# Kernel optimization log

Measured on AMD Instinct MI355X. Metric: run time of the kernel, lower is better.

## Reference

```python
import jax, jax.numpy as jnp
import numpy as np

T, B, D = 512, 16, 1024


def entmax_1_5(x):
    # x: [..., D] fp32. 1.5-entmax via sort + cumsum threshold search.
    x = x - jnp.max(x, axis=-1, keepdims=True)
    x_sorted = jnp.sort(x, axis=-1)[..., ::-1]          # descending
    cumsum = jnp.cumsum(x_sorted, axis=-1)
    d = x.shape[-1]
    k = jnp.arange(1, d + 1, dtype=x.dtype)
    tau = (cumsum - 1.0) / k                             # [..., D]
    support = x_sorted >= tau
    k_star = jnp.clip(jnp.sum(support, axis=-1, keepdims=True), 1, None)
    tau_star = jnp.take_along_axis(tau, k_star - 1, axis=-1)
    p_unnorm = jnp.sqrt(jnp.clip(x - tau_star, 0.0, None))  # (.)**0.5
    return p_unnorm / (jnp.sum(p_unnorm, axis=-1, keepdims=True) + 1e-10)


def setup_inputs() -> dict:
    key = jax.random.key(0)
    k1, k2, k3, k4 = jax.random.split(key, 4)
    x = jax.random.normal(k1, (T, B, D), dtype=jnp.float32)
    z = jax.random.normal(k2, (T, B, D), dtype=jnp.float32)
    h0 = jnp.zeros((B, D), dtype=jnp.float32)
    # parameters (xavier-ish scale for W_x, scaled near-orthogonal-ish for W_h)
    W_x = jax.random.normal(k3, (D, D), dtype=jnp.float32) * (1.0 / np.sqrt(D))
    W_h = jax.random.normal(k4, (D, D), dtype=jnp.float32) * (0.9 / np.sqrt(D))
    b = jnp.zeros((D,), dtype=jnp.float32)
    return {"x": x, "z": z, "h0": h0, "W_x": W_x, "W_h": W_h, "b": b}


def reference(x, z, h0, W_x, W_h, b):
    # gate does not depend on the recurrence -> compute for all T at once
    gate = entmax_1_5(z.astype(jnp.float32)).astype(z.dtype)  # [T,B,D]

    def step(h_prev, x_t):
        h_new = jnp.tanh(x_t @ W_x.T + h_prev @ W_h.T + b)
        return h_new, h_new

    _, hs = jax.lax.scan(step, h0, x)          # hs: [T,B,D]
    h = jnp.concatenate([h0[None], hs], axis=0)  # [T+1,B,D]
    output = hs * gate                           # [T,B,D]
    return (output, h)
```

## Files before the change

kernel.cpp:

```cpp
#include <hip/hip_runtime.h>
#include <math.h>

#define T_STEPS 512
#define BATCH   16
#define DIM     1024
#define M_TOTAL (T_STEPS*BATCH)
#define OUT_SEC ((size_t)M_TOTAL*DIM)
#define BD      (BATCH*DIM)

#define TAG_BYTES ((size_t)2*BD*8)

#define NB_GEMM 512
#define NB_GATE 2048

__device__ __forceinline__ float wred64(float v){
  #pragma unroll
  for (int off = 32; off >= 1; off >>= 1) v += __shfl_xor(v, off, 64);
  return v;
}

#define KA(v) asm volatile("" : "+v"(v.x), "+v"(v.y), "+v"(v.z), "+v"(v.w))

__global__ __launch_bounds__(256) void prep_kernel(const float* __restrict__ X,
                                                   const float* __restrict__ Wx,
                                                   const float* __restrict__ bias,
                                                   float* __restrict__ out_h,
                                                   const float* __restrict__ z,
                                                   float* __restrict__ gate_out){
  __shared__ float As[8][128];
  __shared__ float Bs[8][128];
  const int tid = threadIdx.x;

  if (blockIdx.x < NB_GEMM){
    const int bm = blockIdx.x >> 3;
    const int bn = blockIdx.x & 7;
    const int m0 = bm*128, n0 = bn*128;
    const int tx = tid & 15, ty = tid >> 4;
    const int sm = tid >> 1;
    const int sk = (tid & 1) * 4;

    float acc[8][8] = {};

    for (int k0 = 0; k0 < DIM; k0 += 8){
      const float4 av = *reinterpret_cast<const float4*>(
          X  + (size_t)(m0+sm)*DIM + k0 + sk);
      const float4 wv = *reinterpret_cast<const float4*>(
          Wx + (size_t)(n0+sm)*DIM + k0 + sk);
      __syncthreads();
      As[sk+0][sm]=av.x; As[sk+1][sm]=av.y; As[sk+2][sm]=av.z; As[sk+3][sm]=av.w;
      Bs[sk+0][sm]=wv.x; Bs[sk+1][sm]=wv.y; Bs[sk+2][sm]=wv.z; Bs[sk+3][sm]=wv.w;
      __syncthreads();
      #pragma unroll
      for (int k = 0; k < 8; ++k){
        float af[8], bf[8];
        #pragma unroll
        for (int i = 0; i < 8; ++i) af[i] = As[k][ty + 16*i];
        #pragma unroll
        for (int j = 0; j < 8; ++j) bf[j] = Bs[k][tx + 16*j];
        #pragma unroll
        for (int i = 0; i < 8; ++i)
          #pragma unroll
          for (int j = 0; j < 8; ++j) acc[i][j] = fmaf(af[i], bf[j], acc[i][j]);
      }
    }

    float bv[8];
    #pragma unroll
    for (int j = 0; j < 8; ++j) bv[j] = bias[n0 + tx + 16*j];
    #pragma unroll
    for (int i = 0; i < 8; ++i){
      float* dst = out_h + (size_t)(m0 + ty + 16*i + BATCH)*DIM + n0 + tx;
      #pragma unroll
      for (int j = 0; j < 8; ++j) dst[16*j] = acc[i][j] + bv[j];
    }
  } else {
    const int gb   = blockIdx.x - NB_GEMM;
    const int row  = gb * 4 + (tid >> 6);
    const int lane = tid & 63;
    const float* zr = z + (size_t)row * DIM;

    float x[16];
    #pragma unroll
    for (int e = 0; e < 4; ++e){
      float4 v = *reinterpret_cast<const float4*>(zr + e*256 + lane*4);
      x[e*4+0]=v.x; x[e*4+1]=v.y; x[e*4+2]=v.z; x[e*4+3]=v.w;
    }

    float m = x[0];
    #pragma unroll
    for (int i = 1; i < 16; ++i) m = fmaxf(m, x[i]);
    #pragma unroll
    for (int off = 32; off >= 1; off >>= 1) m = fmaxf(m, __shfl_xor(m, off, 64));

    float lo = m - 1.0f, hi = m;
    for (int it = 0; it < 30; ++it){
      float mid = 0.5f*(lo + hi);
      float f = 0.f;
      #pragma unroll
      for (int i = 0; i < 16; ++i) f += fmaxf(x[i] - mid, 0.f);
      f = wred64(f);
      if (f >= 1.0f) lo = mid; else hi = mid;
    }
    float s = 0.f, kc = 0.f;
    #pragma unroll
    for (int i = 0; i < 16; ++i){ if (x[i] > lo){ s += x[i]; kc += 1.f; } }
    s = wred64(s); kc = wred64(kc);
    const float tau = (s - 1.0f) / kc;

    float p[16]; float ps = 0.f;
    #pragma unroll
    for (int i = 0; i < 16; ++i){ p[i] = sqrtf(fmaxf(x[i] - tau, 0.f)); ps += p[i]; }
    ps = wred64(ps);
    const float inv = 1.0f / (ps + 1e-10f);

    float* go = gate_out + (size_t)row * DIM;
    #pragma unroll
    for (int e = 0; e < 4; ++e){
      float4 v; v.x=p[e*4]*inv; v.y=p[e*4+1]*inv; v.z=p[e*4+2]*inv; v.w=p[e*4+3]*inv;
      *reinterpret_cast<float4*>(go + e*256 + lane*4) = v;
    }
  }
}

__global__ __launch_bounds__(1024, 1) void rnn_tag(const float* __restrict__ h0,
                                                   const float* __restrict__ Wh,
                                                   float* __restrict__ out,
                                                   uint2* __restrict__ tagbuf){
  float* out_h = out + OUT_SEC;
  const int tid  = threadIdx.x;
  const int lane = tid & 63;
  const int w    = tid >> 6;
  const int b    = blockIdx.x >> 4;
  const int s    = blockIdx.x & 15;
  const int dbase = s*64 + w*4;

  __shared__ float hbuf[2][DIM];

  float4 wreg[4][4];
  #pragma unroll
  for (int r = 0; r < 4; ++r)
    #pragma unroll
    for (int j = 0; j < 4; ++j)
      wreg[r][j] = *reinterpret_cast<const float4*>(
          Wh + (size_t)(dbase + r)*DIM + lane*4 + j*256);

  KA(wreg[0][0]); KA(wreg[0][1]); KA(wreg[0][2]); KA(wreg[0][3]);
  KA(wreg[1][0]); KA(wreg[1][1]); KA(wreg[1][2]); KA(wreg[1][3]);
  KA(wreg[2][0]); KA(wreg[2][1]); KA(wreg[2][2]); KA(wreg[2][3]);
  KA(wreg[3][0]); KA(wreg[3][1]); KA(wreg[3][2]); KA(wreg[3][3]);

  if (tid < 16)
    reinterpret_cast<float4*>(out_h + (size_t)b*DIM + s*64)[tid] =
        reinterpret_cast<const float4*>(h0 + (size_t)b*DIM + s*64)[tid];

  const int  myrow  = 2*((lane >> 5) & 1) + ((lane >> 4) & 1);
  const bool active = ((lane & 15) == 0);

  for (int t = 0; t < T_STEPS; ++t){
    float pre_v = 0.f, gate_v = 0.f;
    if (active){
      const size_t d = dbase + myrow;
      pre_v  = out_h[(size_t)(t+1)*BD + (size_t)b*DIM + d];
      gate_v = out  [(size_t)t*BD     + (size_t)b*DIM + d];
    }

    if (t == 0){
      hbuf[0][tid] = h0[(size_t)b*DIM + tid];
    } else {
      const uint2* pp = tagbuf + (size_t)(t & 1)*BD + (size_t)b*DIM + tid;
      const unsigned want = (unsigned)t;
      uint2 q;
      do {
        asm volatile("global_load_dwordx2 %0, %1, off sc0 sc1\n\t"
                     "s_waitcnt vmcnt(0)"
                     : "=&v"(q) : "v"(pp) : "memory");
      } while (q.y != want);
      hbuf[t & 1][tid] = __uint_as_float(q.x);
    }
    __syncthreads();

    const float* src = &hbuf[t & 1][0];
    const float4 hv0 = *reinterpret_cast<const float4*>(src + lane*4);
    const float4 hv1 = *reinterpret_cast<const float4*>(src + 256 + lane*4);
    const float4 hv2 = *reinterpret_cast<const float4*>(src + 512 + lane*4);
    const float4 hv3 = *reinterpret_cast<const float4*>(src + 768 + lane*4);

    float v0,v1,v2,v3;
    {
      #define DOTROW(R, OUTV)                                            \
        { const float4 w0=wreg[R][0], w1=wreg[R][1],                     \
                       w2=wreg[R][2], w3=wreg[R][3];                     \
          float a_ = 0.f;                                                \
          a_ = fmaf(w0.x,hv0.x,fmaf(w0.y,hv0.y,fmaf(w0.z,hv0.z,fmaf(w0.w,hv0.w,a_)))); \
          a_ = fmaf(w1.x,hv1.x,fmaf(w1.y,hv1.y,fmaf(w1.z,hv1.z,fmaf(w1.w,hv1.w,a_)))); \
          a_ = fmaf(w2.x,hv2.x,fmaf(w2.y,hv2.y,fmaf(w2.z,hv2.z,fmaf(w2.w,hv2.w,a_)))); \
          a_ = fmaf(w3.x,hv3.x,fmaf(w3.y,hv3.y,fmaf(w3.z,hv3.z,fmaf(w3.w,hv3.w,a_)))); \
          OUTV = a_; }
      DOTROW(0,v0) DOTROW(1,v1) DOTROW(2,v2) DOTROW(3,v3)
      #undef DOTROW
    }

    const bool sA = (lane & 32) != 0;
    float a0 = (sA? v2 : v0) + __shfl_xor(sA? v0 : v2, 32, 64);
    float a1 = (sA? v3 : v1) + __shfl_xor(sA? v1 : v3, 32, 64);
    const bool sB = (lane & 16) != 0;
    float c0 = (sB? a1 : a0) + __shfl_xor(sB? a0 : a1, 16, 64);
    c0 += __shfl_xor(c0, 8, 64);
    c0 += __shfl_xor(c0, 4, 64);
    c0 += __shfl_xor(c0, 2, 64);
    c0 += __shfl_xor(c0, 1, 64);

    if (active){
      const float v  = pre_v + c0;
      const float e  = __expf(2.0f * v);
      const float hn = 1.0f - 2.0f / (e + 1.0f);
      const size_t d = dbase + myrow;
      if (t != T_STEPS - 1){
        const unsigned long long pkt =
            ((unsigned long long)(unsigned)(t + 1) << 32) |
            (unsigned long long)__float_as_uint(hn);
        __hip_atomic_store(
            reinterpret_cast<unsigned long long*>(
                tagbuf + (size_t)((t + 1) & 1)*BD + (size_t)b*DIM + d),
            pkt, __ATOMIC_RELAXED, __HIP_MEMORY_SCOPE_AGENT);
      }
      out_h[(size_t)(t+1)*BD + (size_t)b*DIM + d] = hn;
      out  [(size_t)t*BD     + (size_t)b*DIM + d] = hn * gate_v;
    }
  }
}

extern "C" void kernel_launch(void* const* d_in, const int* in_sizes, int n_in,
                              void* d_out, int out_size, void* d_ws, size_t ws_size,
                              hipStream_t stream){
  (void)in_sizes; (void)n_in; (void)out_size; (void)ws_size;
  const float* x    = (const float*)d_in[0];
  const float* z    = (const float*)d_in[1];
  const float* h0   = (const float*)d_in[2];
  const float* Wx   = (const float*)d_in[3];
  const float* Wh   = (const float*)d_in[4];
  const float* bias = (const float*)d_in[5];
  float* out   = (float*)d_out;
  float* out_h = out + OUT_SEC;

  hipMemsetAsync(d_ws, 0, TAG_BYTES, stream);
  prep_kernel<<<NB_GEMM + NB_GATE, 256, 0, stream>>>(x, Wx, bias, out_h, z, out);
  rnn_tag    <<<256, 1024, 0, stream>>>(h0, Wh, out, (uint2*)d_ws);
}
```

Measured before the change: 1.147 ms.

## Process two batches per RNN block with 512 threads and prefetch GEMM tiles

The recurrent kernel now has each 512-thread block handle 32 output rows for two batch elements, interleaved, instead of 64 rows for one batch. Each block reuses its register-resident W_h slice across both batches and polls tags with 16-byte loads covering two elements per thread. While step t for batch A is finished, step t for batch B can overlap with tag propagation, which may hide cross-block latency. The cost is a longer serial chain per step in each block, a single hbuf per batch with no double buffer, and a possible race when the next step's writes land before slow warps finish reading. The prep GEMM also prefetches the next k-tile from global memory before computing on the current one.

```diff
diff --git a/kernel.cpp b/kernel.cpp
--- a/kernel.cpp
+++ b/kernel.cpp
@@ -41,14 +41,19 @@
 
     float acc[8][8] = {};
 
+    const float* Xp = X  + (size_t)(m0+sm)*DIM + sk;
+    const float* Wp = Wx + (size_t)(n0+sm)*DIM + sk;
+
+    float4 av = *reinterpret_cast<const float4*>(Xp);
+    float4 wv = *reinterpret_cast<const float4*>(Wp);
+
     for (int k0 = 0; k0 < DIM; k0 += 8){
-      const float4 av = *reinterpret_cast<const float4*>(
-          X  + (size_t)(m0+sm)*DIM + k0 + sk);
-      const float4 wv = *reinterpret_cast<const float4*>(
-          Wx + (size_t)(n0+sm)*DIM + k0 + sk);
       __syncthreads();
       As[sk+0][sm]=av.x; As[sk+1][sm]=av.y; As[sk+2][sm]=av.z; As[sk+3][sm]=av.w;
       Bs[sk+0][sm]=wv.x; Bs[sk+1][sm]=wv.y; Bs[sk+2][sm]=wv.z; Bs[sk+3][sm]=wv.w;
+      const int kn = (k0 + 8 < DIM) ? (k0 + 8) : 0;
+      const float4 av2 = *reinterpret_cast<const float4*>(Xp + kn);
+      const float4 wv2 = *reinterpret_cast<const float4*>(Wp + kn);
       __syncthreads();
       #pragma unroll
       for (int k = 0; k < 8; ++k){
@@ -62,6 +67,7 @@
           #pragma unroll
           for (int j = 0; j < 8; ++j) acc[i][j] = fmaf(af[i], bf[j], acc[i][j]);
       }
+      av = av2; wv = wv2;
     }
 
     float bv[8];
@@ -122,19 +128,97 @@
   }
 }
 
-__global__ __launch_bounds__(1024, 1) void rnn_tag(const float* __restrict__ h0,
-                                                   const float* __restrict__ Wh,
-                                                   float* __restrict__ out,
-                                                   uint2* __restrict__ tagbuf){
+__device__ __forceinline__ void rnn_seg(int t, int b, float* __restrict__ hbuf,
+    const float* __restrict__ h0, float* __restrict__ out,
+    float* __restrict__ out_h, uint2* __restrict__ tagbuf,
+    const float4 (&wreg)[4][4],
+    int tid, int lane, int dbase, int myrow, bool active)
+{
+  float pre_v = 0.f, gate_v = 0.f;
+  if (active){
+    const size_t d = dbase + myrow;
+    pre_v  = out_h[(size_t)(t+1)*BD + (size_t)b*DIM + d];
+    gate_v = out  [(size_t)t*BD     + (size_t)b*DIM + d];
+  }
+
+  if (t == 0){
+    const float2 hl = *reinterpret_cast<const float2*>(h0 + (size_t)b*DIM + 2*tid);
+    *reinterpret_cast<float2*>(&hbuf[2*tid]) = hl;
+  } else {
+    const uint2* pp = tagbuf + (size_t)(t & 1)*BD + (size_t)b*DIM + 2*tid;
+    const unsigned want = (unsigned)t;
+    float4 q;
+    do {
+      asm volatile("global_load_dwordx4 %0, %1, off sc0 sc1\n\t"
+                   "s_waitcnt vmcnt(0)"
+                   : "=&v"(q) : "v"(pp) : "memory");
+    } while (__float_as_uint(q.y) != want || __float_as_uint(q.w) != want);
+    *reinterpret_cast<float2*>(&hbuf[2*tid]) = make_float2(q.x, q.z);
+  }
+  __syncthreads();
+
+  const float4 hv0 = *reinterpret_cast<const float4*>(hbuf + lane*4);
+  const float4 hv1 = *reinterpret_cast<const float4*>(hbuf + 256 + lane*4);
+  const float4 hv2 = *reinterpret_cast<const float4*>(hbuf + 512 + lane*4);
+  const float4 hv3 = *reinterpret_cast<const float4*>(hbuf + 768 + lane*4);
+
+  float v0,v1,v2,v3;
+  #define DOTROW(R, OUTV)                                            \
+    { const float4 w0=wreg[R][0], w1=wreg[R][1],                     \
+                   w2=wreg[R][2], w3=wreg[R][3];                     \
+      float a_ = 0.f;                                                \
+      a_ = fmaf(w0.x,hv0.x,fmaf(w0.y,hv0.y,fmaf(w0.z,hv0.z,fmaf(w0.w,hv0.w,a_)))); \
+      a_ = fmaf(w1.x,hv1.x,fmaf(w1.y,hv1.y,fmaf(w1.z,hv1.z,fmaf(w1.w,hv1.w,a_)))); \
+      a_ = fmaf(w2.x,hv2.x,fmaf(w2.y,hv2.y,fmaf(w2.z,hv2.z,fmaf(w2.w,hv2.w,a_)))); \
+      a_ = fmaf(w3.x,hv3.x,fmaf(w3.y,hv3.y,fmaf(w3.z,hv3.z,fmaf(w3.w,hv3.w,a_)))); \
+      OUTV = a_; }
+  DOTROW(0,v0) DOTROW(1,v1) DOTROW(2,v2) DOTROW(3,v3)
+  #undef DOTROW
+
+  const bool sA = (lane & 32) != 0;
+  float a0 = (sA? v2 : v0) + __shfl_xor(sA? v0 : v2, 32, 64);
+  float a1 = (sA? v3 : v1) + __shfl_xor(sA? v1 : v3, 32, 64);
+  const bool sB = (lane & 16) != 0;
+  float c0 = (sB? a1 : a0) + __shfl_xor(sB? a0 : a1, 16, 64);
+  c0 += __shfl_xor(c0, 8, 64);
+  c0 += __shfl_xor(c0, 4, 64);
+  c0 += __shfl_xor(c0, 2, 64);
+  c0 += __shfl_xor(c0, 1, 64);
+
+  if (active){
+    const float v  = pre_v + c0;
+    const float e  = __expf(2.0f * v);
+    const float hn = 1.0f - 2.0f / (e + 1.0f);
+    const size_t d = dbase + myrow;
+    if (t != T_STEPS - 1){
+      const unsigned long long pkt =
+          ((unsigned long long)(unsigned)(t + 1) << 32) |
+          (unsigned long long)__float_as_uint(hn);
+      __hip_atomic_store(
+          reinterpret_cast<unsigned long long*>(
+              tagbuf + (size_t)((t + 1) & 1)*BD + (size_t)b*DIM + d),
+          pkt, __ATOMIC_RELAXED, __HIP_MEMORY_SCOPE_AGENT);
+    }
+    out_h[(size_t)(t+1)*BD + (size_t)b*DIM + d] = hn;
+    out  [(size_t)t*BD     + (size_t)b*DIM + d] = hn * gate_v;
+  }
+}
+
+__global__ __launch_bounds__(512, 1) void rnn_tag(const float* __restrict__ h0,
+                                                  const float* __restrict__ Wh,
+                                                  float* __restrict__ out,
+                                                  uint2* __restrict__ tagbuf){
   float* out_h = out + OUT_SEC;
   const int tid  = threadIdx.x;
   const int lane = tid & 63;
   const int w    = tid >> 6;
-  const int b    = blockIdx.x >> 4;
-  const int s    = blockIdx.x & 15;
-  const int dbase = s*64 + w*4;
-
-  __shared__ float hbuf[2][DIM];
+  const int bp   = blockIdx.x >> 5;
+  const int s    = blockIdx.x & 31;
+  const int bA   = 2*bp, bB = 2*bp + 1;
+  const int dbase = s*32 + w*4;
+
+  __shared__ float hbufA[DIM];
+  __shared__ float hbufB[DIM];
 
   float4 wreg[4][4];
   #pragma unroll
@@ -149,84 +233,21 @@
   KA(wreg[2][0]); KA(wreg[2][1]); KA(wreg[2][2]); KA(wreg[2][3]);
   KA(wreg[3][0]); KA(wreg[3][1]); KA(wreg[3][2]); KA(wreg[3][3]);
 
-  if (tid < 16)
-    reinterpret_cast<float4*>(out_h + (size_t)b*DIM + s*64)[tid] =
-        reinterpret_cast<const float4*>(h0 + (size_t)b*DIM + s*64)[tid];
+  if (tid < 8)
+    reinterpret_cast<float4*>(out_h + (size_t)bA*DIM + s*32)[tid] =
+        reinterpret_cast<const float4*>(h0 + (size_t)bA*DIM + s*32)[tid];
+  else if (tid < 16)
+    reinterpret_cast<float4*>(out_h + (size_t)bB*DIM + s*32)[tid - 8] =
+        reinterpret_cast<const float4*>(h0 + (size_t)bB*DIM + s*32)[tid - 8];
 
   const int  myrow  = 2*((lane >> 5) & 1) + ((lane >> 4) & 1);
   const bool active = ((lane & 15) == 0);
 
   for (int t = 0; t < T_STEPS; ++t){
-    float pre_v = 0.f, gate_v = 0.f;
-    if (active){
-      const size_t d = dbase + myrow;
-      pre_v  = out_h[(size_t)(t+1)*BD + (size_t)b*DIM + d];
-      gate_v = out  [(size_t)t*BD     + (size_t)b*DIM + d];
-    }
-
-    if (t == 0){
-      hbuf[0][tid] = h0[(size_t)b*DIM + tid];
-    } else {
-      const uint2* pp = tagbuf + (size_t)(t & 1)*BD + (size_t)b*DIM + tid;
-      const unsigned want = (unsigned)t;
-      uint2 q;
-      do {
-        asm volatile("global_load_dwordx2 %0, %1, off sc0 sc1\n\t"
-                     "s_waitcnt vmcnt(0)"
-                     : "=&v"(q) : "v"(pp) : "memory");
-      } while (q.y != want);
-      hbuf[t & 1][tid] = __uint_as_float(q.x);
-    }
-    __syncthreads();
-
-    const float* src = &hbuf[t & 1][0];
-    const float4 hv0 = *reinterpret_cast<const float4*>(src + lane*4);
-    const float4 hv1 = *reinterpret_cast<const float4*>(src + 256 + lane*4);
-    const float4 hv2 = *reinterpret_cast<const float4*>(src + 512 + lane*4);
-    const float4 hv3 = *reinterpret_cast<const float4*>(src + 768 + lane*4);
-
-    float v0,v1,v2,v3;
-    {
-      #define DOTROW(R, OUTV)                                            \
-        { const float4 w0=wreg[R][0], w1=wreg[R][1],                     \
-                       w2=wreg[R][2], w3=wreg[R][3];                     \
-          float a_ = 0.f;                                                \
-          a_ = fmaf(w0.x,hv0.x,fmaf(w0.y,hv0.y,fmaf(w0.z,hv0.z,fmaf(w0.w,hv0.w,a_)))); \
-          a_ = fmaf(w1.x,hv1.x,fmaf(w1.y,hv1.y,fmaf(w1.z,hv1.z,fmaf(w1.w,hv1.w,a_)))); \
-          a_ = fmaf(w2.x,hv2.x,fmaf(w2.y,hv2.y,fmaf(w2.z,hv2.z,fmaf(w2.w,hv2.w,a_)))); \
-          a_ = fmaf(w3.x,hv3.x,fmaf(w3.y,hv3.y,fmaf(w3.z,hv3.z,fmaf(w3.w,hv3.w,a_)))); \
-          OUTV = a_; }
-      DOTROW(0,v0) DOTROW(1,v1) DOTROW(2,v2) DOTROW(3,v3)
-      #undef DOTROW
-    }
-
-    const bool sA = (lane & 32) != 0;
-    float a0 = (sA? v2 : v0) + __shfl_xor(sA? v0 : v2, 32, 64);
-    float a1 = (sA? v3 : v1) + __shfl_xor(sA? v1 : v3, 32, 64);
-    const bool sB = (lane & 16) != 0;
-    float c0 = (sB? a1 : a0) + __shfl_xor(sB? a0 : a1, 16, 64);
-    c0 += __shfl_xor(c0, 8, 64);
-    c0 += __shfl_xor(c0, 4, 64);
-    c0 += __shfl_xor(c0, 2, 64);
-    c0 += __shfl_xor(c0, 1, 64);
-
-    if (active){
-      const float v  = pre_v + c0;
-      const float e  = __expf(2.0f * v);
-      const float hn = 1.0f - 2.0f / (e + 1.0f);
-      const size_t d = dbase + myrow;
-      if (t != T_STEPS - 1){
-        const unsigned long long pkt =
-            ((unsigned long long)(unsigned)(t + 1) << 32) |
-            (unsigned long long)__float_as_uint(hn);
-        __hip_atomic_store(
-            reinterpret_cast<unsigned long long*>(
-                tagbuf + (size_t)((t + 1) & 1)*BD + (size_t)b*DIM + d),
-            pkt, __ATOMIC_RELAXED, __HIP_MEMORY_SCOPE_AGENT);
-      }
-      out_h[(size_t)(t+1)*BD + (size_t)b*DIM + d] = hn;
-      out  [(size_t)t*BD     + (size_t)b*DIM + d] = hn * gate_v;
-    }
+    rnn_seg(t, bA, hbufA, h0, out, out_h, tagbuf, wreg,
+            tid, lane, dbase, myrow, active);
+    rnn_seg(t, bB, hbufB, h0, out, out_h, tagbuf, wreg,
+            tid, lane, dbase, myrow, active);
   }
 }
 
@@ -245,5 +266,5 @@
 
   hipMemsetAsync(d_ws, 0, TAG_BYTES, stream);
   prep_kernel<<<NB_GEMM + NB_GATE, 256, 0, stream>>>(x, Wx, bias, out_h, z, out);
-  rnn_tag    <<<256, 1024, 0, stream>>>(h0, Wh, out, (uint2*)d_ws);
-}
+  rnn_tag    <<<256, 512, 0, stream>>>(h0, Wh, out, (uint2*)d_ws);
+}
```

Result: slower. 1.400 ms (+22.0%).
